# Kernel tuning notes

Measured on AMD Instinct MI355X. Metric: run time of the kernel, lower is better.

The kernel has to match this reference:

```python
import jax, jax.numpy as jnp
import numpy as np

N, T, H = 4000, 32, 64      # N = batch_size*n_neurons, t_repetition, gcn_d
E = 1024000
NT = N * T                   # graph nodes after temporal unrolling
N_NEURONS = 500
B = N // N_NEURONS
T_EBD = 16                   # tau * t_repetition = 0.5*32
N_STEPS = 12


def setup_inputs() -> dict:
    key = jax.random.key(0)
    ks = jax.random.split(key, 13)
    s = 1.0 / np.sqrt(H)
    return {
        "node_features": jax.random.normal(ks[0], (N, T, H), jnp.float32),
        "edge_index_batch": jax.random.randint(ks[1], (2, E), 0, NT, jnp.int32),
        "edge_attr_batch": jax.random.uniform(ks[2], (E,), jnp.float32),
        "batch": jax.random.randint(ks[3], (N,), 0, B, jnp.int32),
        # GRU params (1 layer, torch layout: W_ih [3H,H], W_hh [3H,H])
        "gru_Wih": jax.random.normal(ks[4], (3 * H, H), jnp.float32) * s,
        "gru_Whh": jax.random.normal(ks[5], (3 * H, H), jnp.float32) * s,
        "gru_bih": jax.random.normal(ks[6], (3 * H,), jnp.float32) * s,
        "gru_bhh": jax.random.normal(ks[7], (3 * H,), jnp.float32) * s,
        # GCNConv linear weight [out,in], no bias
        "gcn_W": jax.random.normal(ks[8], (H, H), jnp.float32) * s,
        # temporal attention MLP: Linear(T->T_ebd), Linear(T_ebd->T), no bias
        "attn_W1": jax.random.normal(ks[9], (T_EBD, T), jnp.float32) * (1.0 / np.sqrt(T)),
        "attn_W2": jax.random.normal(ks[10], (T, T_EBD), jnp.float32) * (1.0 / np.sqrt(T_EBD)),
        # final head Linear(gcn_d -> n_steps) with bias
        "fc_W": jax.random.normal(ks[11], (N_STEPS, H), jnp.float32) * s,
        "fc_b": jax.random.normal(ks[12], (N_STEPS,), jnp.float32) * s,
    }


def _gru(x, Wih, Whh, bih, bhh):
    # x: [N, T, H] -> outputs [N, T, H] (torch GRU equations, h0 = 0)
    xg = x @ Wih.T + bih  # [N, T, 3H], input projection precomputed

    def step(h, xg_t):
        hg = h @ Whh.T + bhh
        xr, xz, xn = jnp.split(xg_t, 3, axis=-1)
        hr, hz, hn = jnp.split(hg, 3, axis=-1)
        r = jax.nn.sigmoid(xr + hr)
        z = jax.nn.sigmoid(xz + hz)
        n = jnp.tanh(xn + r * hn)
        h_new = (1.0 - z) * n + z * h
        return h_new, h_new

    h0 = jnp.zeros((x.shape[0], Whh.shape[1]), x.dtype)
    _, hs = jax.lax.scan(step, h0, jnp.swapaxes(xg, 0, 1))  # hs: [T, N, H]
    return jnp.swapaxes(hs, 0, 1)


def _gcn(x, W, edge_index, edge_weight, n_nodes):
    # PyG GCNConv: add self-loops (weight 1), symmetric deg^-1/2 norm, no bias
    loops = jnp.arange(n_nodes, dtype=edge_index.dtype)
    src = jnp.concatenate([edge_index[0], loops])
    dst = jnp.concatenate([edge_index[1], loops])
    w = jnp.concatenate([edge_weight, jnp.ones((n_nodes,), edge_weight.dtype)])
    xw = x @ W.T                                            # [NT, H]
    deg = jax.ops.segment_sum(w, dst, num_segments=n_nodes)
    dis = jnp.where(deg > 0, jax.lax.rsqrt(jnp.where(deg > 0, deg, 1.0)), 0.0)
    norm = dis[src] * w * dis[dst]                          # [E+NT]
    msgs = norm[:, None] * xw[src]                          # gather + scale
    return jax.ops.segment_sum(msgs, dst, num_segments=n_nodes)


def reference(node_features, edge_index_batch, edge_attr_batch, batch,
              gru_Wih, gru_Whh, gru_bih, gru_bhh, gcn_W,
              attn_W1, attn_W2, fc_W, fc_b):
    # DGRLayer: GRU over time, then GCN over the flattened (node,time) graph
    g = _gru(node_features, gru_Wih, gru_Whh, gru_bih, gru_bhh)  # [N, T, H]
    x = g.reshape(NT, H)
    x = _gcn(x, gcn_W, edge_index_batch, edge_attr_batch, NT)
    x3 = x.reshape(N, T, H)

    # TemporalAttention (reshape mirrors torch contiguous .view semantics)
    xt = x3.reshape(B, T, N_NEURONS * H).mean(axis=-1)           # [B, T]
    attn = jax.nn.sigmoid(jax.nn.relu(xt @ attn_W1.T) @ attn_W2.T)  # [B, T]

    nf = x3.reshape(B, T, N_NEURONS, H)
    pooled = jnp.sum(attn[:, :, None, None] * nf, axis=(1, 2))   # [B, H]
    return pooled @ fc_W.T + fc_b                                # [B, n_steps]
```

## Files before the change

kernel.cpp:

```cpp
#include <hip/hip_runtime.h>
#include <hip/hip_fp16.h>

#define NNODES   4000
#define TSTEPS   32
#define HDIM     64
#define ECOUNT   1024000
#define NTOT     128000
#define BATCHB   8
#define NNEUR    500
#define TEBD     16
#define NSTEPS   12

#define CNT_SHIFT 23
#define SUM_MASK  0x7FFFFFu
#define SUM_SCALE 262144.0f
#define SLOTS     32
#define REC_BLOCKS (NNODES / 16)

#define ROWS_PER_WAVE  5
#define ROWS_PER_BLOCK 20

typedef _Float16 half8_t __attribute__((ext_vector_type(8)));
typedef float    f32x4_t __attribute__((ext_vector_type(4)));

__device__ __forceinline__ float sigmoidf_(float x) {
    return 1.0f / (1.0f + __expf(-x));
}
__device__ __forceinline__ float tanhf_(float x) {
    return 1.0f - 2.0f / (1.0f + __expf(2.0f * x));
}

__global__ __launch_bounds__(256) void k_recHist(
    const float* __restrict__ x, const float* __restrict__ Wih,
    const float* __restrict__ Whh, const float* __restrict__ bih,
    const float* __restrict__ bhh, const float* __restrict__ Wg,
    _Float16* __restrict__ xwh,
    const int* __restrict__ ei, const float* __restrict__ ea,
    unsigned* __restrict__ dc, int2* __restrict__ se32)
{
    __shared__ __align__(16) _Float16 hbuf[2][16 * 72];

    const int tid = threadIdx.x;

    if (blockIdx.x >= REC_BLOCKS) {
        int e = (blockIdx.x - REC_BLOCKS) * 256 + tid;
        int s = ei[e], d = ei[ECOUNT + e];
        float w = ea[e];
        unsigned fx = (unsigned)(w * SUM_SCALE + 0.5f);
        unsigned old = atomicAdd(&dc[d], (1u << CNT_SHIFT) | fx);
        int r = (int)(old >> CNT_SHIFT);
        if (r < SLOTS)
            se32[d * SLOTS + r] = make_int2(s, __float_as_int(w));
        return;
    }

    const int lane = tid & 63;
    const int wv   = tid >> 6;
    const int c    = lane & 15;
    const int quad = lane >> 4;
    const int n0   = blockIdx.x * 16;

    auto makeB = [&](const float* W, int row, int k0) -> half8_t {
        const float4* p = (const float4*)(W + (size_t)row * HDIM + k0);
        float4 u = p[0], v = p[1];
        half8_t h;
        h[0] = (_Float16)u.x; h[1] = (_Float16)u.y; h[2] = (_Float16)u.z; h[3] = (_Float16)u.w;
        h[4] = (_Float16)v.x; h[5] = (_Float16)v.y; h[6] = (_Float16)v.z; h[7] = (_Float16)v.w;
        return h;
    };

    half8_t Bxr[2], Bxz[2], Bxn[2], Bhr[2], Bhz[2], Bhn[2], Bw[2];
#pragma unroll
    for (int kt = 0; kt < 2; ++kt) {
        int k0 = kt * 32 + quad * 8;
        Bxr[kt] = makeB(Wih, wv * 16 + c, k0);
        Bxz[kt] = makeB(Wih, 64 + wv * 16 + c, k0);
        Bxn[kt] = makeB(Wih, 128 + wv * 16 + c, k0);
        Bhr[kt] = makeB(Whh, wv * 16 + c, k0);
        Bhz[kt] = makeB(Whh, 64 + wv * 16 + c, k0);
        Bhn[kt] = makeB(Whh, 128 + wv * 16 + c, k0);
        Bw[kt]  = makeB(Wg, wv * 16 + c, k0);
    }

    const int f = wv * 16 + c;
    const float brz_r = bih[f] + bhh[f];
    const float brz_z = bih[64 + f] + bhh[64 + f];
    const float bin_  = bih[128 + f];
    const float bhn_  = bhh[128 + f];

    float hreg[4] = {0.f, 0.f, 0.f, 0.f};
    half8_t ah[2];

    const float* xp = x + (size_t)(n0 + c) * (TSTEPS * HDIM) + quad * 8;

    float4 xq0[4], xq1[4];
    {
        const float* p0 = xp;
        xq0[0] = *(const float4*)(p0);      xq0[1] = *(const float4*)(p0 + 4);
        xq0[2] = *(const float4*)(p0 + 32); xq0[3] = *(const float4*)(p0 + 36);
        const float* p1 = xp + HDIM;
        xq1[0] = *(const float4*)(p1);      xq1[1] = *(const float4*)(p1 + 4);
        xq1[2] = *(const float4*)(p1 + 32); xq1[3] = *(const float4*)(p1 + 36);
    }

    auto step = [&](int t, float4* xq) {
        half8_t ax[2];
#pragma unroll
        for (int kt = 0; kt < 2; ++kt) {
            float4 u = xq[kt * 2], v = xq[kt * 2 + 1];
            half8_t a;
            a[0] = (_Float16)u.x; a[1] = (_Float16)u.y; a[2] = (_Float16)u.z; a[3] = (_Float16)u.w;
            a[4] = (_Float16)v.x; a[5] = (_Float16)v.y; a[6] = (_Float16)v.z; a[7] = (_Float16)v.w;
            ax[kt] = a;
        }
        if (t + 2 < TSTEPS) {
            const float* pt = xp + (size_t)(t + 2) * HDIM;
            xq[0] = *(const float4*)(pt);      xq[1] = *(const float4*)(pt + 4);
            xq[2] = *(const float4*)(pt + 32); xq[3] = *(const float4*)(pt + 36);
        }

        f32x4_t Cr  = (f32x4_t){0.f, 0.f, 0.f, 0.f};
        f32x4_t Cz  = (f32x4_t){0.f, 0.f, 0.f, 0.f};
        f32x4_t Cnx = (f32x4_t){0.f, 0.f, 0.f, 0.f};
        f32x4_t Cnh = (f32x4_t){0.f, 0.f, 0.f, 0.f};

#pragma unroll
        for (int kt = 0; kt < 2; ++kt) {
            Cr  = __builtin_amdgcn_mfma_f32_16x16x32_f16(ax[kt], Bxr[kt], Cr, 0, 0, 0);
            Cz  = __builtin_amdgcn_mfma_f32_16x16x32_f16(ax[kt], Bxz[kt], Cz, 0, 0, 0);
            Cnx = __builtin_amdgcn_mfma_f32_16x16x32_f16(ax[kt], Bxn[kt], Cnx, 0, 0, 0);
        }
        if (t > 0) {
#pragma unroll
            for (int kt = 0; kt < 2; ++kt) {
                Cr  = __builtin_amdgcn_mfma_f32_16x16x32_f16(ah[kt], Bhr[kt], Cr, 0, 0, 0);
                Cz  = __builtin_amdgcn_mfma_f32_16x16x32_f16(ah[kt], Bhz[kt], Cz, 0, 0, 0);
                Cnh = __builtin_amdgcn_mfma_f32_16x16x32_f16(ah[kt], Bhn[kt], Cnh, 0, 0, 0);
            }
        }

        _Float16* hb = hbuf[t & 1];
#pragma unroll
        for (int r = 0; r < 4; ++r) {
            float rr = sigmoidf_(Cr[r] + brz_r);
            float zz = sigmoidf_(Cz[r] + brz_z);
            float nn = tanhf_(Cnx[r] + bin_ + rr * (Cnh[r] + bhn_));
            float hn = (1.0f - zz) * nn + zz * hreg[r];
            hreg[r] = hn;
            hb[(quad * 4 + r) * 72 + f] = (_Float16)hn;
        }

        __syncthreads();

#pragma unroll
        for (int kt = 0; kt < 2; ++kt)
            ah[kt] = *(half8_t*)&hb[c * 72 + kt * 32 + quad * 8];

        f32x4_t Cw = (f32x4_t){0.f, 0.f, 0.f, 0.f};
#pragma unroll
        for (int kt = 0; kt < 2; ++kt)
            Cw = __builtin_amdgcn_mfma_f32_16x16x32_f16(ah[kt], Bw[kt], Cw, 0, 0, 0);

#pragma unroll
        for (int r = 0; r < 4; ++r) {
            int row = (n0 + quad * 4 + r) * TSTEPS + t;
            xwh[(size_t)row * HDIM + f] = (_Float16)Cw[r];
        }
    };

#pragma unroll 1
    for (int tt = 0; tt < TSTEPS; tt += 2) {
        step(tt, xq0);
        step(tt + 1, xq1);
    }
}

__global__ __launch_bounds__(256) void k_gather(
    const _Float16* __restrict__ xwh, const unsigned* __restrict__ dc,
    const int2* __restrict__ se32, float* __restrict__ S)
{
    const int tid  = threadIdx.x;
    const int lane = tid & 63;
    const int wv   = tid >> 6;
    const int d0   = blockIdx.x * ROWS_PER_BLOCK + wv * ROWS_PER_WAVE;

    unsigned pk[ROWS_PER_WAVE];
    float    sf[ROWS_PER_WAVE];
#pragma unroll
    for (int i = 0; i < ROWS_PER_WAVE; ++i) pk[i] = dc[d0 + i];
#pragma unroll
    for (int i = 0; i < ROWS_PER_WAVE; ++i)
        sf[i] = (float)xwh[(size_t)(d0 + i) * HDIM + lane];

    float acc = 0.f;
#pragma unroll
    for (int i = 0; i < ROWS_PER_WAVE; ++i) {
        const int d = d0 + i;
        const float dd = rsqrtf(1.0f + (float)(pk[i] & SUM_MASK) * 0x1p-18f);
        int cnt = (int)(pk[i] >> CNT_SHIFT);
        cnt = cnt < SLOTS ? cnt : SLOTS;
        const int2* bkt = se32 + (size_t)d * SLOTS;

        float a0 = dd * sf[i];
        float a1 = 0.f, a2 = 0.f, a3 = 0.f;
        int j = 0;
        for (; j + 4 <= cnt; j += 4) {
            int2 e0 = bkt[j], e1 = bkt[j + 1], e2 = bkt[j + 2], e3 = bkt[j + 3];
            unsigned p0 = dc[e0.x], p1 = dc[e1.x];
            unsigned p2 = dc[e2.x], p3 = dc[e3.x];
            float c0 = rsqrtf(1.0f + (float)(p0 & SUM_MASK) * 0x1p-18f) * __int_as_float(e0.y);
            float c1 = rsqrtf(1.0f + (float)(p1 & SUM_MASK) * 0x1p-18f) * __int_as_float(e1.y);
            float c2 = rsqrtf(1.0f + (float)(p2 & SUM_MASK) * 0x1p-18f) * __int_as_float(e2.y);
            float c3 = rsqrtf(1.0f + (float)(p3 & SUM_MASK) * 0x1p-18f) * __int_as_float(e3.y);
            float v0 = (float)xwh[(size_t)e0.x * HDIM + lane];
            float v1 = (float)xwh[(size_t)e1.x * HDIM + lane];
            float v2 = (float)xwh[(size_t)e2.x * HDIM + lane];
            float v3 = (float)xwh[(size_t)e3.x * HDIM + lane];
            a0 = fmaf(c0, v0, a0);
            a1 = fmaf(c1, v1, a1);
            a2 = fmaf(c2, v2, a2);
            a3 = fmaf(c3, v3, a3);
        }
        for (; j < cnt; ++j) {
            int2 e = bkt[j];
            unsigned pe = dc[e.x];
            a0 = fmaf(rsqrtf(1.0f + (float)(pe & SUM_MASK) * 0x1p-18f) * __int_as_float(e.y),
                      (float)xwh[(size_t)e.x * HDIM + lane], a0);
        }
        acc = fmaf(dd, (a0 + a1) + (a2 + a3), acc);
    }

    __shared__ float red[256];
    red[tid] = acc;
    __syncthreads();
    if (tid < 64) {
        float s = red[tid] + red[64 + tid] + red[128 + tid] + red[192 + tid];
        atomicAdd(&S[((blockIdx.x * ROWS_PER_BLOCK) / NNEUR) * HDIM + tid], s);
    }
}

__global__ __launch_bounds__(256) void k_final(
    const float* __restrict__ S, const float* __restrict__ W1,
    const float* __restrict__ W2, const float* __restrict__ fcW,
    const float* __restrict__ fcb, float* __restrict__ out)
{
    __shared__ float xt[256];
    __shared__ float a1[128];
    __shared__ float attn[256];
    __shared__ float pooled[512];
    const int tid = threadIdx.x;

    {
        float s = 0.f;
        const float* p = S + tid * 64;
#pragma unroll
        for (int hh = 0; hh < 64; ++hh) s += p[hh];
        xt[tid] = s * (1.0f / 32000.0f);
    }
    __syncthreads();
    if (tid < 128) {
        int b = tid >> 4, i = tid & 15;
        float s = 0.f;
#pragma unroll
        for (int t = 0; t < 32; ++t) s += xt[b * 32 + t] * W1[i * 32 + t];
        a1[tid] = fmaxf(s, 0.f);
    }
    __syncthreads();
    {
        int b = tid >> 5, t = tid & 31;
        float s = 0.f;
#pragma unroll
        for (int i = 0; i < 16; ++i) s += a1[b * 16 + i] * W2[t * 16 + i];
        attn[tid] = 1.0f / (1.0f + __expf(-s));
    }
    __syncthreads();
    for (int o = tid; o < 512; o += 256) {
        int b = o >> 6, h = o & 63;
        float s = 0.f;
#pragma unroll
        for (int t = 0; t < 32; ++t) s += attn[b * 32 + t] * S[(b * 32 + t) * 64 + h];
        pooled[o] = s;
    }
    __syncthreads();
    if (tid < BATCHB * NSTEPS) {
        int b = tid / NSTEPS, st = tid % NSTEPS;
        float acc = fcb[st];
#pragma unroll
        for (int h = 0; h < 64; ++h) acc += pooled[b * 64 + h] * fcW[st * 64 + h];
        out[b * NSTEPS + st] = acc;
    }
}

extern "C" void kernel_launch(void* const* d_in, const int* in_sizes, int n_in,
                              void* d_out, int out_size, void* d_ws, size_t ws_size,
                              hipStream_t stream) {
    const float* x   = (const float*)d_in[0];
    const int*   ei  = (const int*)  d_in[1];
    const float* ea  = (const float*)d_in[2];
    const float* Wih = (const float*)d_in[4];
    const float* Whh = (const float*)d_in[5];
    const float* bih = (const float*)d_in[6];
    const float* bhh = (const float*)d_in[7];
    const float* Wg  = (const float*)d_in[8];
    const float* W1  = (const float*)d_in[9];
    const float* W2  = (const float*)d_in[10];
    const float* fcW = (const float*)d_in[11];
    const float* fcb = (const float*)d_in[12];
    float* out = (float*)d_out;

    char* p = (char*)d_ws;
    unsigned* dc = (unsigned*)p;   p += sizeof(unsigned) * NTOT;
    float* S = (float*)p;          p += sizeof(float) * 256 * HDIM;
    int2*  se32 = (int2*)p;        p += sizeof(int2) * (size_t)NTOT * SLOTS;
    _Float16* xwh = (_Float16*)p;  p += sizeof(_Float16) * (size_t)NTOT * HDIM;

    hipMemsetAsync(dc, 0, sizeof(unsigned) * NTOT + sizeof(float) * 256 * HDIM, stream);
    k_recHist <<<REC_BLOCKS + ECOUNT / 256, 256, 0, stream>>>(
        x, Wih, Whh, bih, bhh, Wg, xwh, ei, ea, dc, se32);
    k_gather  <<<NTOT / ROWS_PER_BLOCK, 256, 0, stream>>>(xwh, dc, se32, S);
    k_final   <<<1, 256, 0, stream>>>(S, W1, W2, fcW, fcb, out);
}
```

Baseline: 236.5 us.

## Pack edge buckets into 32-bit words and fuse final head into gather kernel

```diff
diff --git a/kernel.cpp b/kernel.cpp
--- a/kernel.cpp
+++ b/kernel.cpp
@@ -16,9 +16,11 @@
 #define SUM_SCALE 262144.0f
 #define SLOTS     32
 #define REC_BLOCKS (NNODES / 16)
+#define HIST_BLOCKS (ECOUNT / 512)
 
 #define ROWS_PER_WAVE  5
 #define ROWS_PER_BLOCK 20
+#define GATHER_BLOCKS  (NTOT / ROWS_PER_BLOCK)
 
 typedef _Float16 half8_t __attribute__((ext_vector_type(8)));
 typedef float    f32x4_t __attribute__((ext_vector_type(4)));
@@ -36,21 +38,28 @@
     const float* __restrict__ bhh, const float* __restrict__ Wg,
     _Float16* __restrict__ xwh,
     const int* __restrict__ ei, const float* __restrict__ ea,
-    unsigned* __restrict__ dc, int2* __restrict__ se32)
+    unsigned* __restrict__ dc, unsigned* __restrict__ se32)
 {
     __shared__ __align__(16) _Float16 hbuf[2][16 * 72];
 
     const int tid = threadIdx.x;
 
     if (blockIdx.x >= REC_BLOCKS) {
-        int e = (blockIdx.x - REC_BLOCKS) * 256 + tid;
-        int s = ei[e], d = ei[ECOUNT + e];
-        float w = ea[e];
-        unsigned fx = (unsigned)(w * SUM_SCALE + 0.5f);
-        unsigned old = atomicAdd(&dc[d], (1u << CNT_SHIFT) | fx);
-        int r = (int)(old >> CNT_SHIFT);
-        if (r < SLOTS)
-            se32[d * SLOTS + r] = make_int2(s, __float_as_int(w));
+        int e0 = (blockIdx.x - REC_BLOCKS) * 512 + tid;
+        int e1 = e0 + 256;
+        int s0 = ei[e0],          s1 = ei[e1];
+        int d0 = ei[ECOUNT + e0], d1 = ei[ECOUNT + e1];
+        float w0 = ea[e0],        w1 = ea[e1];
+        unsigned q0 = (unsigned)(w0 * 32768.0f + 0.5f); q0 = q0 > 32767u ? 32767u : q0;
+        unsigned q1 = (unsigned)(w1 * 32768.0f + 0.5f); q1 = q1 > 32767u ? 32767u : q1;
+        unsigned fx0 = (unsigned)(w0 * SUM_SCALE + 0.5f);
+        unsigned fx1 = (unsigned)(w1 * SUM_SCALE + 0.5f);
+        unsigned old0 = atomicAdd(&dc[d0], (1u << CNT_SHIFT) | fx0);
+        unsigned old1 = atomicAdd(&dc[d1], (1u << CNT_SHIFT) | fx1);
+        int r0 = (int)(old0 >> CNT_SHIFT);
+        int r1 = (int)(old1 >> CNT_SHIFT);
+        if (r0 < SLOTS) se32[d0 * SLOTS + r0] = ((unsigned)s0 << 15) | q0;
+        if (r1 < SLOTS) se32[d1 * SLOTS + r1] = ((unsigned)s1 << 15) | q1;
         return;
     }
 
@@ -175,9 +184,13 @@
     }
 }
 
-__global__ __launch_bounds__(256) void k_gather(
+__global__ __launch_bounds__(256) void k_gatherFinal(
     const _Float16* __restrict__ xwh, const unsigned* __restrict__ dc,
-    const int2* __restrict__ se32, float* __restrict__ S)
+    const unsigned* __restrict__ se32, float* __restrict__ S,
+    unsigned* __restrict__ fin,
+    const float* __restrict__ W1, const float* __restrict__ W2,
+    const float* __restrict__ fcW, const float* __restrict__ fcb,
+    float* __restrict__ out)
 {
     const int tid  = threadIdx.x;
     const int lane = tid & 63;
@@ -199,33 +212,35 @@
         const float dd = rsqrtf(1.0f + (float)(pk[i] & SUM_MASK) * 0x1p-18f);
         int cnt = (int)(pk[i] >> CNT_SHIFT);
         cnt = cnt < SLOTS ? cnt : SLOTS;
-        const int2* bkt = se32 + (size_t)d * SLOTS;
+        const unsigned* bkt = se32 + (size_t)d * SLOTS;
 
         float a0 = dd * sf[i];
         float a1 = 0.f, a2 = 0.f, a3 = 0.f;
         int j = 0;
         for (; j + 4 <= cnt; j += 4) {
-            int2 e0 = bkt[j], e1 = bkt[j + 1], e2 = bkt[j + 2], e3 = bkt[j + 3];
-            unsigned p0 = dc[e0.x], p1 = dc[e1.x];
-            unsigned p2 = dc[e2.x], p3 = dc[e3.x];
-            float c0 = rsqrtf(1.0f + (float)(p0 & SUM_MASK) * 0x1p-18f) * __int_as_float(e0.y);
-            float c1 = rsqrtf(1.0f + (float)(p1 & SUM_MASK) * 0x1p-18f) * __int_as_float(e1.y);
-            float c2 = rsqrtf(1.0f + (float)(p2 & SUM_MASK) * 0x1p-18f) * __int_as_float(e2.y);
-            float c3 = rsqrtf(1.0f + (float)(p3 & SUM_MASK) * 0x1p-18f) * __int_as_float(e3.y);
-            float v0 = (float)xwh[(size_t)e0.x * HDIM + lane];
-            float v1 = (float)xwh[(size_t)e1.x * HDIM + lane];
-            float v2 = (float)xwh[(size_t)e2.x * HDIM + lane];
-            float v3 = (float)xwh[(size_t)e3.x * HDIM + lane];
+            uint4 q = *(const uint4*)(bkt + j);
+            int s0 = (int)(q.x >> 15), s1 = (int)(q.y >> 15);
+            int s2 = (int)(q.z >> 15), s3 = (int)(q.w >> 15);
+            unsigned p0 = dc[s0], p1 = dc[s1], p2 = dc[s2], p3 = dc[s3];
+            float c0 = rsqrtf(1.0f + (float)(p0 & SUM_MASK) * 0x1p-18f) * ((float)(q.x & 0x7FFFu) * 0x1p-15f);
+            float c1 = rsqrtf(1.0f + (float)(p1 & SUM_MASK) * 0x1p-18f) * ((float)(q.y & 0x7FFFu) * 0x1p-15f);
+            float c2 = rsqrtf(1.0f + (float)(p2 & SUM_MASK) * 0x1p-18f) * ((float)(q.z & 0x7FFFu) * 0x1p-15f);
+            float c3 = rsqrtf(1.0f + (float)(p3 & SUM_MASK) * 0x1p-18f) * ((float)(q.w & 0x7FFFu) * 0x1p-15f);
+            float v0 = (float)xwh[(size_t)s0 * HDIM + lane];
+            float v1 = (float)xwh[(size_t)s1 * HDIM + lane];
+            float v2 = (float)xwh[(size_t)s2 * HDIM + lane];
+            float v3 = (float)xwh[(size_t)s3 * HDIM + lane];
             a0 = fmaf(c0, v0, a0);
             a1 = fmaf(c1, v1, a1);
             a2 = fmaf(c2, v2, a2);
             a3 = fmaf(c3, v3, a3);
         }
         for (; j < cnt; ++j) {
-            int2 e = bkt[j];
-            unsigned pe = dc[e.x];
-            a0 = fmaf(rsqrtf(1.0f + (float)(pe & SUM_MASK) * 0x1p-18f) * __int_as_float(e.y),
-                      (float)xwh[(size_t)e.x * HDIM + lane], a0);
+            unsigned u = bkt[j];
+            int s = (int)(u >> 15);
+            unsigned pe = dc[s];
+            a0 = fmaf(rsqrtf(1.0f + (float)(pe & SUM_MASK) * 0x1p-18f) * ((float)(u & 0x7FFFu) * 0x1p-15f),
+                      (float)xwh[(size_t)s * HDIM + lane], a0);
         }
         acc = fmaf(dd, (a0 + a1) + (a2 + a3), acc);
     }
@@ -237,24 +252,30 @@
         float s = red[tid] + red[64 + tid] + red[128 + tid] + red[192 + tid];
         atomicAdd(&S[((blockIdx.x * ROWS_PER_BLOCK) / NNEUR) * HDIM + tid], s);
     }
-}
-
-__global__ __launch_bounds__(256) void k_final(
-    const float* __restrict__ S, const float* __restrict__ W1,
-    const float* __restrict__ W2, const float* __restrict__ fcW,
-    const float* __restrict__ fcb, float* __restrict__ out)
-{
+
+    __threadfence();
+    __shared__ int lastFlag;
+    __syncthreads();
+    if (tid == 0) {
+        unsigned prev = atomicAdd(fin, 1u);
+        lastFlag = (prev == GATHER_BLOCKS - 1);
+    }
+    __syncthreads();
+    if (!lastFlag) return;
+
+    auto ldS = [&](int i) -> float {
+        return __hip_atomic_load(&S[i], __ATOMIC_RELAXED, __HIP_MEMORY_SCOPE_AGENT);
+    };
+
     __shared__ float xt[256];
-    __shared__ float a1[128];
+    __shared__ float a1s[128];
     __shared__ float attn[256];
     __shared__ float pooled[512];
-    const int tid = threadIdx.x;
 
     {
         float s = 0.f;
-        const float* p = S + tid * 64;
-#pragma unroll
-        for (int hh = 0; hh < 64; ++hh) s += p[hh];
+#pragma unroll
+        for (int hh = 0; hh < 64; ++hh) s += ldS(tid * 64 + hh);
         xt[tid] = s * (1.0f / 32000.0f);
     }
     __syncthreads();
@@ -263,14 +284,14 @@
         float s = 0.f;
 #pragma unroll
         for (int t = 0; t < 32; ++t) s += xt[b * 32 + t] * W1[i * 32 + t];
-        a1[tid] = fmaxf(s, 0.f);
+        a1s[tid] = fmaxf(s, 0.f);
     }
     __syncthreads();
     {
         int b = tid >> 5, t = tid & 31;
         float s = 0.f;
 #pragma unroll
-        for (int i = 0; i < 16; ++i) s += a1[b * 16 + i] * W2[t * 16 + i];
+        for (int i = 0; i < 16; ++i) s += a1s[b * 16 + i] * W2[t * 16 + i];
         attn[tid] = 1.0f / (1.0f + __expf(-s));
     }
     __syncthreads();
@@ -278,16 +299,16 @@
         int b = o >> 6, h = o & 63;
         float s = 0.f;
 #pragma unroll
-        for (int t = 0; t < 32; ++t) s += attn[b * 32 + t] * S[(b * 32 + t) * 64 + h];
+        for (int t = 0; t < 32; ++t) s += attn[b * 32 + t] * ldS((b * 32 + t) * 64 + h);
         pooled[o] = s;
     }
     __syncthreads();
     if (tid < BATCHB * NSTEPS) {
         int b = tid / NSTEPS, st = tid % NSTEPS;
-        float acc = fcb[st];
-#pragma unroll
-        for (int h = 0; h < 64; ++h) acc += pooled[b * 64 + h] * fcW[st * 64 + h];
-        out[b * NSTEPS + st] = acc;
+        float acc2 = fcb[st];
+#pragma unroll
+        for (int h = 0; h < 64; ++h) acc2 += pooled[b * 64 + h] * fcW[st * 64 + h];
+        out[b * NSTEPS + st] = acc2;
     }
 }
 
@@ -311,12 +332,13 @@
     char* p = (char*)d_ws;
     unsigned* dc = (unsigned*)p;   p += sizeof(unsigned) * NTOT;
     float* S = (float*)p;          p += sizeof(float) * 256 * HDIM;
-    int2*  se32 = (int2*)p;        p += sizeof(int2) * (size_t)NTOT * SLOTS;
+    unsigned* fin = (unsigned*)p;  p += 16;
+    unsigned* se32 = (unsigned*)p; p += sizeof(unsigned) * (size_t)NTOT * SLOTS;
     _Float16* xwh = (_Float16*)p;  p += sizeof(_Float16) * (size_t)NTOT * HDIM;
 
-    hipMemsetAsync(dc, 0, sizeof(unsigned) * NTOT + sizeof(float) * 256 * HDIM, stream);
-    k_recHist <<<REC_BLOCKS + ECOUNT / 256, 256, 0, stream>>>(
+    hipMemsetAsync(dc, 0, sizeof(unsigned) * NTOT + sizeof(float) * 256 * HDIM + 16, stream);
+    k_recHist <<<REC_BLOCKS + HIST_BLOCKS, 256, 0, stream>>>(
         x, Wih, Whh, bih, bhh, Wg, xwh, ei, ea, dc, se32);
-    k_gather  <<<NTOT / ROWS_PER_BLOCK, 256, 0, stream>>>(xwh, dc, se32, S);
-    k_final   <<<1, 256, 0, stream>>>(S, W1, W2, fcW, fcb, out);
-}
+    k_gatherFinal <<<GATHER_BLOCKS, 256, 0, stream>>>(
+        xwh, dc, se32, S, fin, W1, W2, fcW, fcb, out);
+}
```

Result: slower. 846.7 us (+258.0%).

## Pre-scale features by source degree and pack edge records into 32 bits

Applied to the files above, without the earlier changes.

```diff
diff --git a/kernel.cpp b/kernel.cpp
--- a/kernel.cpp
+++ b/kernel.cpp
@@ -15,10 +15,13 @@
 #define SUM_MASK  0x7FFFFFu
 #define SUM_SCALE 262144.0f
 #define SLOTS     32
-#define REC_BLOCKS (NNODES / 16)
+#define REC_BLOCKS  (NNODES / 16)
+#define HIST_BLOCKS (ECOUNT / 256)
+#define SCALE_BLOCKS (NTOT * HDIM / 8 / 256)
 
 #define ROWS_PER_WAVE  5
 #define ROWS_PER_BLOCK 20
+#define GATHER_BLOCKS  (NTOT / ROWS_PER_BLOCK)
 
 typedef _Float16 half8_t __attribute__((ext_vector_type(8)));
 typedef float    f32x4_t __attribute__((ext_vector_type(4)));
@@ -36,7 +39,7 @@
     const float* __restrict__ bhh, const float* __restrict__ Wg,
     _Float16* __restrict__ xwh,
     const int* __restrict__ ei, const float* __restrict__ ea,
-    unsigned* __restrict__ dc, int2* __restrict__ se32)
+    unsigned* __restrict__ dc, unsigned* __restrict__ se32)
 {
     __shared__ __align__(16) _Float16 hbuf[2][16 * 72];
 
@@ -46,11 +49,12 @@
         int e = (blockIdx.x - REC_BLOCKS) * 256 + tid;
         int s = ei[e], d = ei[ECOUNT + e];
         float w = ea[e];
+        unsigned q = (unsigned)(w * 32768.0f + 0.5f); q = q > 32767u ? 32767u : q;
         unsigned fx = (unsigned)(w * SUM_SCALE + 0.5f);
         unsigned old = atomicAdd(&dc[d], (1u << CNT_SHIFT) | fx);
         int r = (int)(old >> CNT_SHIFT);
         if (r < SLOTS)
-            se32[d * SLOTS + r] = make_int2(s, __float_as_int(w));
+            se32[d * SLOTS + r] = ((unsigned)s << 15) | q;
         return;
     }
 
@@ -175,9 +179,21 @@
     }
 }
 
+__global__ __launch_bounds__(256) void k_scale(
+    _Float16* __restrict__ xwh, const unsigned* __restrict__ dc)
+{
+    const int t = blockIdx.x * 256 + threadIdx.x;
+    const int row = t >> 3;
+    const float dd = rsqrtf(1.0f + (float)(dc[row] & SUM_MASK) * 0x1p-18f);
+    half8_t v = *(half8_t*)&xwh[(size_t)t * 8];
+#pragma unroll
+    for (int i = 0; i < 8; ++i) v[i] = (_Float16)((float)v[i] * dd);
+    *(half8_t*)&xwh[(size_t)t * 8] = v;
+}
+
 __global__ __launch_bounds__(256) void k_gather(
-    const _Float16* __restrict__ xwh, const unsigned* __restrict__ dc,
-    const int2* __restrict__ se32, float* __restrict__ S)
+    const _Float16* __restrict__ xws, const unsigned* __restrict__ dc,
+    const unsigned* __restrict__ se32, float* __restrict__ S)
 {
     const int tid  = threadIdx.x;
     const int lane = tid & 63;
@@ -190,7 +206,7 @@
     for (int i = 0; i < ROWS_PER_WAVE; ++i) pk[i] = dc[d0 + i];
 #pragma unroll
     for (int i = 0; i < ROWS_PER_WAVE; ++i)
-        sf[i] = (float)xwh[(size_t)(d0 + i) * HDIM + lane];
+        sf[i] = (float)xws[(size_t)(d0 + i) * HDIM + lane];
 
     float acc = 0.f;
 #pragma unroll
@@ -199,33 +215,46 @@
         const float dd = rsqrtf(1.0f + (float)(pk[i] & SUM_MASK) * 0x1p-18f);
         int cnt = (int)(pk[i] >> CNT_SHIFT);
         cnt = cnt < SLOTS ? cnt : SLOTS;
-        const int2* bkt = se32 + (size_t)d * SLOTS;
-
-        float a0 = dd * sf[i];
+        const unsigned* bkt = se32 + (size_t)d * SLOTS;
+
+        float a0 = sf[i];
         float a1 = 0.f, a2 = 0.f, a3 = 0.f;
         int j = 0;
+        for (; j + 8 <= cnt; j += 8) {
+            uint4 qa = *(const uint4*)(bkt + j);
+            uint4 qb = *(const uint4*)(bkt + j + 4);
+            float v0 = (float)xws[(size_t)(qa.x >> 15) * HDIM + lane];
+            float v1 = (float)xws[(size_t)(qa.y >> 15) * HDIM + lane];
+            float v2 = (float)xws[(size_t)(qa.z >> 15) * HDIM + lane];
+            float v3 = (float)xws[(size_t)(qa.w >> 15) * HDIM + lane];
+            float v4 = (float)xws[(size_t)(qb.x >> 15) * HDIM + lane];
+            float v5 = (float)xws[(size_t)(qb.y >> 15) * HDIM + lane];
+            float v6 = (float)xws[(size_t)(qb.z >> 15) * HDIM + lane];
+            float v7 = (float)xws[(size_t)(qb.w >> 15) * HDIM + lane];
+            a0 = fmaf((float)(qa.x & 0x7FFFu) * 0x1p-15f, v0, a0);
+            a1 = fmaf((float)(qa.y & 0x7FFFu) * 0x1p-15f, v1, a1);
+            a2 = fmaf((float)(qa.z & 0x7FFFu) * 0x1p-15f, v2, a2);
+            a3 = fmaf((float)(qa.w & 0x7FFFu) * 0x1p-15f, v3, a3);
+            a0 = fmaf((float)(qb.x & 0x7FFFu) * 0x1p-15f, v4, a0);
+            a1 = fmaf((float)(qb.y & 0x7FFFu) * 0x1p-15f, v5, a1);
+            a2 = fmaf((float)(qb.z & 0x7FFFu) * 0x1p-15f, v6, a2);
+            a3 = fmaf((float)(qb.w & 0x7FFFu) * 0x1p-15f, v7, a3);
+        }
         for (; j + 4 <= cnt; j += 4) {
-            int2 e0 = bkt[j], e1 = bkt[j + 1], e2 = bkt[j + 2], e3 = bkt[j + 3];
-            unsigned p0 = dc[e0.x], p1 = dc[e1.x];
-            unsigned p2 = dc[e2.x], p3 = dc[e3.x];
-            float c0 = rsqrtf(1.0f + (float)(p0 & SUM_MASK) * 0x1p-18f) * __int_as_float(e0.y);
-            float c1 = rsqrtf(1.0f + (float)(p1 & SUM_MASK) * 0x1p-18f) * __int_as_float(e1.y);
-            float c2 = rsqrtf(1.0f + (float)(p2 & SUM_MASK) * 0x1p-18f) * __int_as_float(e2.y);
-            float c3 = rsqrtf(1.0f + (float)(p3 & SUM_MASK) * 0x1p-18f) * __int_as_float(e3.y);
-            float v0 = (float)xwh[(size_t)e0.x * HDIM + lane];
-            float v1 = (float)xwh[(size_t)e1.x * HDIM + lane];
-            float v2 = (float)xwh[(size_t)e2.x * HDIM + lane];
-            float v3 = (float)xwh[(size_t)e3.x * HDIM + lane];
-            a0 = fmaf(c0, v0, a0);
-            a1 = fmaf(c1, v1, a1);
-            a2 = fmaf(c2, v2, a2);
-            a3 = fmaf(c3, v3, a3);
+            uint4 q = *(const uint4*)(bkt + j);
+            float v0 = (float)xws[(size_t)(q.x >> 15) * HDIM + lane];
+            float v1 = (float)xws[(size_t)(q.y >> 15) * HDIM + lane];
+            float v2 = (float)xws[(size_t)(q.z >> 15) * HDIM + lane];
+            float v3 = (float)xws[(size_t)(q.w >> 15) * HDIM + lane];
+            a0 = fmaf((float)(q.x & 0x7FFFu) * 0x1p-15f, v0, a0);
+            a1 = fmaf((float)(q.y & 0x7FFFu) * 0x1p-15f, v1, a1);
+            a2 = fmaf((float)(q.z & 0x7FFFu) * 0x1p-15f, v2, a2);
+            a3 = fmaf((float)(q.w & 0x7FFFu) * 0x1p-15f, v3, a3);
         }
         for (; j < cnt; ++j) {
-            int2 e = bkt[j];
-            unsigned pe = dc[e.x];
-            a0 = fmaf(rsqrtf(1.0f + (float)(pe & SUM_MASK) * 0x1p-18f) * __int_as_float(e.y),
-                      (float)xwh[(size_t)e.x * HDIM + lane], a0);
+            unsigned u = bkt[j];
+            a0 = fmaf((float)(u & 0x7FFFu) * 0x1p-15f,
+                      (float)xws[(size_t)(u >> 15) * HDIM + lane], a0);
         }
         acc = fmaf(dd, (a0 + a1) + (a2 + a3), acc);
     }
@@ -311,12 +340,13 @@
     char* p = (char*)d_ws;
     unsigned* dc = (unsigned*)p;   p += sizeof(unsigned) * NTOT;
     float* S = (float*)p;          p += sizeof(float) * 256 * HDIM;
-    int2*  se32 = (int2*)p;        p += sizeof(int2) * (size_t)NTOT * SLOTS;
+    unsigned* se32 = (unsigned*)p; p += sizeof(unsigned) * (size_t)NTOT * SLOTS;
     _Float16* xwh = (_Float16*)p;  p += sizeof(_Float16) * (size_t)NTOT * HDIM;
 
     hipMemsetAsync(dc, 0, sizeof(unsigned) * NTOT + sizeof(float) * 256 * HDIM, stream);
-    k_recHist <<<REC_BLOCKS + ECOUNT / 256, 256, 0, stream>>>(
+    k_recHist <<<REC_BLOCKS + HIST_BLOCKS, 256, 0, stream>>>(
         x, Wih, Whh, bih, bhh, Wg, xwh, ei, ea, dc, se32);
-    k_gather  <<<NTOT / ROWS_PER_BLOCK, 256, 0, stream>>>(xwh, dc, se32, S);
+    k_scale   <<<SCALE_BLOCKS, 256, 0, stream>>>(xwh, dc);
+    k_gather  <<<GATHER_BLOCKS, 256, 0, stream>>>(xwh, dc, se32, S);
     k_final   <<<1, 256, 0, stream>>>(S, W1, W2, fcW, fcb, out);
 }
```

Result: faster. 228.9 us (-3.2%).
